# Performance work log

Hardware: AMD Instinct MI355X
Metric: run time of the kernel (lower is better)

The kernel has to match this reference:

```python
import jax, jax.numpy as jnp
import numpy as np

# TDNN with context [-2, 2], full_context=True -> kernel_width 5.
# The original per-timestep index_select + tiny conv1d loop is, for full context,
# exactly a single VALID 1D convolution over time, followed by ReLU.

B, T, D_IN, D_OUT, KW = 32, 1024, 512, 512, 5


def setup_inputs() -> dict:
    key = jax.random.key(0)
    k1, k2, k3 = jax.random.split(key, 3)
    stdv = 1.0 / np.sqrt(D_IN)
    x = jax.random.normal(k1, (B, T, D_IN), dtype=jnp.float32)
    kernel = jax.random.normal(k2, (D_OUT, D_IN, KW), dtype=jnp.float32) * stdv
    bias = jax.random.normal(k3, (D_OUT,), dtype=jnp.float32) * stdv
    return {"x": x, "kernel": kernel, "bias": bias}


def reference(x, kernel, bias):
    # x: [B, T, D_in] -> [B, D_in, T] to match torch conv1d layout
    xc = jnp.transpose(x, (0, 2, 1))
    # VALID conv over time; kernel layout OIW matches torch (out, in, width)
    out = jax.lax.conv_general_dilated(
        xc, kernel,
        window_strides=(1,),
        padding="VALID",
        dimension_numbers=("NCW", "OIW", "NCW"),
    )  # [B, D_out, T - KW + 1]
    out = out + bias[None, :, None]
    return jax.nn.relu(out)
```

## Files before the change

kernel.cpp:

```cpp
#include <hip/hip_runtime.h>
#include <stdint.h>

#define BATCH 32
#define TLEN  1024
#define DIN   512
#define DOUT  512
#define KW    5
#define TOUT  1020
#define KDIM  (DIN * KW)

#define BM 256
#define BN 256
#define BK 64
#define NT (KDIM / BK)
#define TILE_E (BM * BK)

typedef __attribute__((ext_vector_type(8))) short bf16x8;
typedef __attribute__((ext_vector_type(4))) float f32x4;

__device__ __forceinline__ uint16_t f2bf(float f) {
    uint32_t u = __float_as_uint(f);
    uint32_t r = u + 0x7FFFu + ((u >> 16) & 1u);
    return (uint16_t)(r >> 16);
}

__global__ void __launch_bounds__(256)
convert_pack(const float4* __restrict__ x, uint4* __restrict__ xb,
             const float* __restrict__ w, uint16_t* __restrict__ wb) {
    const int tid = threadIdx.x;

    for (int u = blockIdx.x; u < 8192; u += 1024) {
        int idx = u * 256 + tid;
        float4 a = x[2 * idx];
        float4 b = x[2 * idx + 1];
        uint4 v;
        v.x = (uint32_t)f2bf(a.x) | ((uint32_t)f2bf(a.y) << 16);
        v.y = (uint32_t)f2bf(a.z) | ((uint32_t)f2bf(a.w) << 16);
        v.z = (uint32_t)f2bf(b.x) | ((uint32_t)f2bf(b.y) << 16);
        v.w = (uint32_t)f2bf(b.z) | ((uint32_t)f2bf(b.w) << 16);
        xb[idx] = v;
    }

    __shared__ float4 lw4[320];
    float* lw = (float*)lw4;
    const int o = blockIdx.x >> 1;
    const int h = blockIdx.x & 1;
    const float4* src = (const float4*)(w + (size_t)o * KDIM + h * 1280);
    #pragma unroll
    for (int j = tid; j < 320; j += 256) lw4[j] = src[j];
    __syncthreads();
    #pragma unroll
    for (int k = 0; k < KW; ++k)
        wb[(size_t)o * KDIM + k * DIN + h * 256 + tid] = f2bf(lw[tid * 5 + k]);
}


#define STAGE_A(buf_, mh_, kt_) do {                                           \
    const uint16_t* lb_ = As_ + (buf_) * TILE_E + (mh_) * 8192;                \
    _Pragma("unroll")                                                          \
    for (int ii = 0; ii < 2; ++ii) {                                          \
        int c_  = ii * 512 + w * 64 + lane;                                   \
        int rh_ = c_ >> 3;                                                    \
        int g_  = (c_ & 7) ^ (rh_ & 7);                                       \
        int gr_ = ((rh_ >> 6) << 7) + (mh_) * 64 + (rh_ & 63);                \
        const uint16_t* gp_ = xrow + (size_t)gr_ * DIN + (kt_) * BK + g_ * 8; \
        const uint16_t* lp_ = lb_ + (ii * 512 + w * 64) * 8;                  \
        __builtin_amdgcn_global_load_lds(                                     \
            (const __attribute__((address_space(1))) void*)gp_,               \
            (__attribute__((address_space(3))) void*)lp_, 16, 0, 0);          \
    }                                                                          \
} while (0)

#define STAGE_B(buf_, nh_, kt_) do {                                           \
    const uint16_t* lb_ = Bs_ + (buf_) * TILE_E + (nh_) * 8192;                \
    _Pragma("unroll")                                                          \
    for (int ii = 0; ii < 2; ++ii) {                                          \
        int c_  = ii * 512 + w * 64 + lane;                                   \
        int rh_ = c_ >> 3;                                                    \
        int g_  = (c_ & 7) ^ (rh_ & 7);                                       \
        int gr_ = ((rh_ >> 5) << 6) + (nh_) * 32 + (rh_ & 31);                \
        const uint16_t* gp_ = wrow + (size_t)gr_ * KDIM + (kt_) * BK + g_ * 8;\
        const uint16_t* lp_ = lb_ + (ii * 512 + w * 64) * 8;                  \
        __builtin_amdgcn_global_load_lds(                                     \
            (const __attribute__((address_space(1))) void*)gp_,               \
            (__attribute__((address_space(3))) void*)lp_, 16, 0, 0);          \
    }                                                                          \
} while (0)

#define LDA(buf_, mh_) do {                                                    \
    const uint16_t* Ab_ = As_ + (buf_) * TILE_E;                               \
    _Pragma("unroll")                                                          \
    for (int mi = 0; mi < 4; ++mi) {                                          \
        int r_ = (mh_) * 128 + wm * 64 + mi * 16 + ml;                        \
        _Pragma("unroll")                                                      \
        for (int h2 = 0; h2 < 2; ++h2) {                                     \
            int cc_ = h2 * 4 + kg;                                            \
            af[mi][h2] = *(const bf16x8*)&Ab_[r_ * BK + ((cc_ ^ (r_ & 7)) * 8)];\
        }                                                                      \
    }                                                                          \
} while (0)

#define LDB(buf_, nh_) do {                                                    \
    const uint16_t* Bb_ = Bs_ + (buf_) * TILE_E;                               \
    _Pragma("unroll")                                                          \
    for (int ni = 0; ni < 2; ++ni) {                                          \
        int r_ = (nh_) * 128 + wn * 32 + ni * 16 + ml;                        \
        _Pragma("unroll")                                                      \
        for (int h2 = 0; h2 < 2; ++h2) {                                     \
            int cc_ = h2 * 4 + kg;                                            \
            bfr[ni][h2] = *(const bf16x8*)&Bb_[r_ * BK + ((cc_ ^ (r_ & 7)) * 8)];\
        }                                                                      \
    }                                                                          \
} while (0)

#define MMA(mh_, nh_) do {                                                     \
    _Pragma("unroll")                                                          \
    for (int h2 = 0; h2 < 2; ++h2)                                            \
        _Pragma("unroll")                                                      \
        for (int mi = 0; mi < 4; ++mi)                                        \
            _Pragma("unroll")                                                  \
            for (int ni = 0; ni < 2; ++ni)                                    \
                acc[(mh_) * 4 + mi][(nh_) * 2 + ni] =                         \
                    __builtin_amdgcn_mfma_f32_16x16x32_bf16(                  \
                        af[mi][h2], bfr[ni][h2],                              \
                        acc[(mh_) * 4 + mi][(nh_) * 2 + ni], 0, 0, 0);        \
} while (0)

#define BARW() do {                                                            \
    __builtin_amdgcn_s_barrier();                                              \
    asm volatile("s_waitcnt lgkmcnt(0)" ::: "memory");                         \
    __builtin_amdgcn_sched_barrier(0);                                         \
} while (0)

#define DO_KTILE(BUF, KT_B, GB, KT_A, GA, VM6)                                 \
       \
    LDA(BUF, 0); LDB(BUF, 0);                                                  \
    if (GB) STAGE_B(1 - (BUF), 0, KT_B);                                       \
    asm volatile("s_waitcnt lgkmcnt(8)" ::: "memory");                         \
    BARW();                                                                    \
    __builtin_amdgcn_s_setprio(1); MMA(0, 0); __builtin_amdgcn_s_setprio(0);   \
    __builtin_amdgcn_s_barrier();                                              \
                                                              \
    LDB(BUF, 1);                                                               \
    if (GA) STAGE_A(BUF, 0, KT_A);                                             \
    BARW();                                                                    \
    __builtin_amdgcn_s_setprio(1); MMA(0, 1); __builtin_amdgcn_s_setprio(0);   \
    __builtin_amdgcn_s_barrier();                                              \
                                                              \
    LDA(BUF, 1);                                                               \
    if (GA) STAGE_B(BUF, 1, KT_A);                                             \
    BARW();                                                                    \
    __builtin_amdgcn_s_setprio(1); MMA(1, 1); __builtin_amdgcn_s_setprio(0);   \
    __builtin_amdgcn_s_barrier();                                              \
                                                              \
    LDB(BUF, 0);                                                               \
    if (GA) STAGE_A(BUF, 1, KT_A);                                             \
    BARW();                                                                    \
    __builtin_amdgcn_s_setprio(1); MMA(1, 0); __builtin_amdgcn_s_setprio(0);   \
    if (VM6) { asm volatile("s_waitcnt vmcnt(6)" ::: "memory"); }              \
    else     { asm volatile("s_waitcnt vmcnt(0)" ::: "memory"); }              \
    __builtin_amdgcn_s_barrier();                                              \
    __builtin_amdgcn_sched_barrier(0);

__global__ void __launch_bounds__(512, 2)
tdnn_gemm(const uint16_t* __restrict__ xb,
          const uint16_t* __restrict__ wb,
          const float* __restrict__ bias,
          float* __restrict__ out) {
    __shared__ uint16_t As_[2 * TILE_E];
    __shared__ uint16_t Bs_[2 * TILE_E];

    const int j  = blockIdx.x;
    const int g  = (j & 7) * 32 + (j >> 3);
    const int mt = g >> 1;
    const int nt = g & 1;
    const int b  = mt >> 2;
    const int t0 = (mt & 3) * BM;
    const int n0 = nt * BN;

    const int tid  = threadIdx.x;
    const int lane = tid & 63;
    const int w    = tid >> 6;
    const int wm   = w >> 2;
    const int wn   = w & 3;
    const int ml   = lane & 15;
    const int kg   = lane >> 4;

    const uint16_t* xrow = xb + (size_t)b * TLEN * DIN + (size_t)t0 * DIN;
    const uint16_t* wrow = wb + (size_t)n0 * KDIM;

    f32x4 acc[8][4] = {};
    bf16x8 af[4][2];
    bf16x8 bfr[2][2];

    STAGE_A(0, 0, 0);
    STAGE_B(0, 0, 0);
    STAGE_A(0, 1, 0);
    STAGE_B(0, 1, 0);
    STAGE_A(1, 0, 1);
    STAGE_B(1, 1, 1);
    STAGE_A(1, 1, 1);
    asm volatile("s_waitcnt vmcnt(6)" ::: "memory");
    __builtin_amdgcn_s_barrier();
    __builtin_amdgcn_sched_barrier(0);

    for (int kt = 0; kt < NT; kt += 2) {
        const bool ga0 = (kt + 2) < NT;
        const bool ga1 = (kt + 3) < NT;
        DO_KTILE(0, kt + 1, true, kt + 2, ga0, ga0)
        DO_KTILE(1, kt + 2, ga0,  kt + 3, ga1, ga1)
    }

    const int rq = (lane >> 4) * 4;
    #pragma unroll
    for (int nf = 0; nf < 4; ++nf) {
        const int o = n0 + wn * 64 + (nf >> 1) * 32 + (nf & 1) * 16 + ml;
        const float bv = bias[o];
        float* orow = out + ((size_t)b * DOUT + o) * TOUT;
        #pragma unroll
        for (int mf = 0; mf < 8; ++mf) {
            const int tb_ = t0 + wm * 128 + (mf >> 2) * 64 + (mf & 3) * 16 + rq;
            if (tb_ + 3 < TOUT) {
                float4 s;
                s.x = fmaxf(acc[mf][nf][0] + bv, 0.0f);
                s.y = fmaxf(acc[mf][nf][1] + bv, 0.0f);
                s.z = fmaxf(acc[mf][nf][2] + bv, 0.0f);
                s.w = fmaxf(acc[mf][nf][3] + bv, 0.0f);
                *(float4*)(orow + tb_) = s;
            }
        }
    }
}

extern "C" void kernel_launch(void* const* d_in, const int* in_sizes, int n_in,
                              void* d_out, int out_size, void* d_ws, size_t ws_size,
                              hipStream_t stream) {
    const float* x    = (const float*)d_in[0];
    const float* wgt  = (const float*)d_in[1];
    const float* bias = (const float*)d_in[2];
    float* out = (float*)d_out;

    uint16_t* xb = (uint16_t*)d_ws;
    uint16_t* wb = (uint16_t*)((char*)d_ws + (size_t)BATCH * TLEN * DIN * 2);

    convert_pack<<<1024, 256, 0, stream>>>((const float4*)x, (uint4*)xb, wgt, wb);
    tdnn_gemm<<<256, 512, 0, stream>>>(xb, wb, bias, out);
}
```

Before: 198.4 us.

## Load weight fragments directly from global into registers, keep only activations in LDS

Weight (B) tiles no longer go through shared memory. Each wave now loads its B fragments straight from global memory into registers. A tiles are still staged in LDS through global_load_lds, with hoisted precomputed addresses and separate A-fragment register sets, and the pipeline is rewritten with an explicit peeled epilogue and retuned vmcnt/lgkmcnt waits. This halves LDS footprint and LDS traffic, which may allow more occupancy and fewer barriers. The cost is uncoalesced, strided global reads of weights per wave, with more register pressure and a higher risk of exposed global latency.

```diff
diff --git a/kernel.cpp b/kernel.cpp
--- a/kernel.cpp
+++ b/kernel.cpp
@@ -13,7 +13,7 @@
 #define BN 256
 #define BK 64
 #define NT (KDIM / BK)
-#define TILE_E (BM * BK)
+#define ATILE_E (BM * BK)
 
 typedef __attribute__((ext_vector_type(8))) short bf16x8;
 typedef __attribute__((ext_vector_type(4))) float f32x4;
@@ -28,7 +28,6 @@
 convert_pack(const float4* __restrict__ x, uint4* __restrict__ xb,
              const float* __restrict__ w, uint16_t* __restrict__ wb) {
     const int tid = threadIdx.x;
-
     for (int u = blockIdx.x; u < 8192; u += 1024) {
         int idx = u * 256 + tid;
         float4 a = x[2 * idx];
@@ -40,7 +39,6 @@
         v.w = (uint32_t)f2bf(b.z) | ((uint32_t)f2bf(b.w) << 16);
         xb[idx] = v;
     }
-
     __shared__ float4 lw4[320];
     float* lw = (float*)lw4;
     const int o = blockIdx.x >> 1;
@@ -55,120 +53,96 @@
 }
 
 
-#define STAGE_A(buf_, mh_, kt_) do {                                           \
-    const uint16_t* lb_ = As_ + (buf_) * TILE_E + (mh_) * 8192;                \
-    _Pragma("unroll")                                                          \
-    for (int ii = 0; ii < 2; ++ii) {                                          \
-        int c_  = ii * 512 + w * 64 + lane;                                   \
-        int rh_ = c_ >> 3;                                                    \
-        int g_  = (c_ & 7) ^ (rh_ & 7);                                       \
-        int gr_ = ((rh_ >> 6) << 7) + (mh_) * 64 + (rh_ & 63);                \
-        const uint16_t* gp_ = xrow + (size_t)gr_ * DIN + (kt_) * BK + g_ * 8; \
-        const uint16_t* lp_ = lb_ + (ii * 512 + w * 64) * 8;                  \
-        __builtin_amdgcn_global_load_lds(                                     \
-            (const __attribute__((address_space(1))) void*)gp_,               \
-            (__attribute__((address_space(3))) void*)lp_, 16, 0, 0);          \
+#define SB() __builtin_amdgcn_sched_barrier(0)
+#define BAR() do { __builtin_amdgcn_s_barrier(); SB(); } while (0)
+#define WAITVM(N) do { asm volatile("s_waitcnt vmcnt(" #N ")" ::: "memory"); SB(); } while (0)
+#define WAITLG(N) do { asm volatile("s_waitcnt lgkmcnt(" #N ")" ::: "memory"); SB(); } while (0)
+
+#define STAGE_A(BUF_, MH_, KT_) do {                                           \
+    _Pragma("unroll")                                                          \
+    for (int ii = 0; ii < 2; ++ii) {                                           \
+        const uint16_t* gp_ = xrow + ab + (MH_) * 32768 + ii * 65536 + (KT_) * 64; \
+        const uint16_t* lp_ = As_ + (BUF_) * ATILE_E + (MH_) * 8192 + ii * 4096 + w * 512; \
+        __builtin_amdgcn_global_load_lds(                                      \
+            (const __attribute__((address_space(1))) void*)gp_,                \
+            (__attribute__((address_space(3))) void*)lp_, 16, 0, 0);           \
     }                                                                          \
 } while (0)
 
-#define STAGE_B(buf_, nh_, kt_) do {                                           \
-    const uint16_t* lb_ = Bs_ + (buf_) * TILE_E + (nh_) * 8192;                \
-    _Pragma("unroll")                                                          \
-    for (int ii = 0; ii < 2; ++ii) {                                          \
-        int c_  = ii * 512 + w * 64 + lane;                                   \
-        int rh_ = c_ >> 3;                                                    \
-        int g_  = (c_ & 7) ^ (rh_ & 7);                                       \
-        int gr_ = ((rh_ >> 5) << 6) + (nh_) * 32 + (rh_ & 31);                \
-        const uint16_t* gp_ = wrow + (size_t)gr_ * KDIM + (kt_) * BK + g_ * 8;\
-        const uint16_t* lp_ = lb_ + (ii * 512 + w * 64) * 8;                  \
-        __builtin_amdgcn_global_load_lds(                                     \
-            (const __attribute__((address_space(1))) void*)gp_,               \
-            (__attribute__((address_space(3))) void*)lp_, 16, 0, 0);          \
+#define DS_AFA(SRC_) do {                                                      \
+    _Pragma("unroll")                                                          \
+    for (int mi = 0; mi < 4; ++mi) {                                           \
+        afA[mi][0] = *(const bf16x8*)&As_[(SRC_) * ATILE_E + mi * 1024 + ae0]; \
+        afA[mi][1] = *(const bf16x8*)&As_[(SRC_) * ATILE_E + mi * 1024 + ae1]; \
     }                                                                          \
 } while (0)
 
-#define LDA(buf_, mh_) do {                                                    \
-    const uint16_t* Ab_ = As_ + (buf_) * TILE_E;                               \
-    _Pragma("unroll")                                                          \
-    for (int mi = 0; mi < 4; ++mi) {                                          \
-        int r_ = (mh_) * 128 + wm * 64 + mi * 16 + ml;                        \
+#define DS_AFB(SRC_) do {                                                      \
+    _Pragma("unroll")                                                          \
+    for (int mi = 0; mi < 4; ++mi) {                                           \
+        afB[mi][0] = *(const bf16x8*)&As_[(SRC_) * ATILE_E + 8192 + mi * 1024 + ae0]; \
+        afB[mi][1] = *(const bf16x8*)&As_[(SRC_) * ATILE_E + 8192 + mi * 1024 + ae1]; \
+    }                                                                          \
+} while (0)
+
+#define GLB_B0(KT_) do {                                                       \
+    bf0[0][0] = *(const bf16x8*)(wrow + bo00 + (KT_) * 64);                    \
+    bf0[0][1] = *(const bf16x8*)(wrow + bo00 + (KT_) * 64 + 32);               \
+    bf0[1][0] = *(const bf16x8*)(wrow + bo01 + (KT_) * 64);                    \
+    bf0[1][1] = *(const bf16x8*)(wrow + bo01 + (KT_) * 64 + 32);               \
+} while (0)
+
+#define GLB_B1(KT_) do {                                                       \
+    bf1[0][0] = *(const bf16x8*)(wrow + bo10 + (KT_) * 64);                    \
+    bf1[0][1] = *(const bf16x8*)(wrow + bo10 + (KT_) * 64 + 32);               \
+    bf1[1][0] = *(const bf16x8*)(wrow + bo11 + (KT_) * 64);                    \
+    bf1[1][1] = *(const bf16x8*)(wrow + bo11 + (KT_) * 64 + 32);               \
+} while (0)
+
+#define MMA(MH_, NH_, AF_, BF_) do {                                           \
+    __builtin_amdgcn_s_setprio(1);                                             \
+    _Pragma("unroll")                                                          \
+    for (int h2 = 0; h2 < 2; ++h2)                                             \
         _Pragma("unroll")                                                      \
-        for (int h2 = 0; h2 < 2; ++h2) {                                     \
-            int cc_ = h2 * 4 + kg;                                            \
-            af[mi][h2] = *(const bf16x8*)&Ab_[r_ * BK + ((cc_ ^ (r_ & 7)) * 8)];\
-        }                                                                      \
-    }                                                                          \
-} while (0)
-
-#define LDB(buf_, nh_) do {                                                    \
-    const uint16_t* Bb_ = Bs_ + (buf_) * TILE_E;                               \
-    _Pragma("unroll")                                                          \
-    for (int ni = 0; ni < 2; ++ni) {                                          \
-        int r_ = (nh_) * 128 + wn * 32 + ni * 16 + ml;                        \
-        _Pragma("unroll")                                                      \
-        for (int h2 = 0; h2 < 2; ++h2) {                                     \
-            int cc_ = h2 * 4 + kg;                                            \
-            bfr[ni][h2] = *(const bf16x8*)&Bb_[r_ * BK + ((cc_ ^ (r_ & 7)) * 8)];\
-        }                                                                      \
-    }                                                                          \
-} while (0)
-
-#define MMA(mh_, nh_) do {                                                     \
-    _Pragma("unroll")                                                          \
-    for (int h2 = 0; h2 < 2; ++h2)                                            \
-        _Pragma("unroll")                                                      \
-        for (int mi = 0; mi < 4; ++mi)                                        \
+        for (int mi = 0; mi < 4; ++mi)                                         \
             _Pragma("unroll")                                                  \
-            for (int ni = 0; ni < 2; ++ni)                                    \
-                acc[(mh_) * 4 + mi][(nh_) * 2 + ni] =                         \
-                    __builtin_amdgcn_mfma_f32_16x16x32_bf16(                  \
-                        af[mi][h2], bfr[ni][h2],                              \
-                        acc[(mh_) * 4 + mi][(nh_) * 2 + ni], 0, 0, 0);        \
-} while (0)
-
-#define BARW() do {                                                            \
-    __builtin_amdgcn_s_barrier();                                              \
-    asm volatile("s_waitcnt lgkmcnt(0)" ::: "memory");                         \
-    __builtin_amdgcn_sched_barrier(0);                                         \
-} while (0)
-
-#define DO_KTILE(BUF, KT_B, GB, KT_A, GA, VM6)                                 \
-       \
-    LDA(BUF, 0); LDB(BUF, 0);                                                  \
-    if (GB) STAGE_B(1 - (BUF), 0, KT_B);                                       \
-    asm volatile("s_waitcnt lgkmcnt(8)" ::: "memory");                         \
-    BARW();                                                                    \
-    __builtin_amdgcn_s_setprio(1); MMA(0, 0); __builtin_amdgcn_s_setprio(0);   \
-    __builtin_amdgcn_s_barrier();                                              \
-                                                              \
-    LDB(BUF, 1);                                                               \
-    if (GA) STAGE_A(BUF, 0, KT_A);                                             \
-    BARW();                                                                    \
-    __builtin_amdgcn_s_setprio(1); MMA(0, 1); __builtin_amdgcn_s_setprio(0);   \
-    __builtin_amdgcn_s_barrier();                                              \
-                                                              \
-    LDA(BUF, 1);                                                               \
-    if (GA) STAGE_B(BUF, 1, KT_A);                                             \
-    BARW();                                                                    \
-    __builtin_amdgcn_s_setprio(1); MMA(1, 1); __builtin_amdgcn_s_setprio(0);   \
-    __builtin_amdgcn_s_barrier();                                              \
-                                                              \
-    LDB(BUF, 0);                                                               \
-    if (GA) STAGE_A(BUF, 1, KT_A);                                             \
-    BARW();                                                                    \
-    __builtin_amdgcn_s_setprio(1); MMA(1, 0); __builtin_amdgcn_s_setprio(0);   \
-    if (VM6) { asm volatile("s_waitcnt vmcnt(6)" ::: "memory"); }              \
-    else     { asm volatile("s_waitcnt vmcnt(0)" ::: "memory"); }              \
-    __builtin_amdgcn_s_barrier();                                              \
-    __builtin_amdgcn_sched_barrier(0);
+            for (int ni = 0; ni < 2; ++ni)                                     \
+                acc[(MH_) * 4 + mi][(NH_) * 2 + ni] =                          \
+                    __builtin_amdgcn_mfma_f32_16x16x32_bf16(                   \
+                        AF_[mi][h2], BF_[ni][h2],                              \
+                        acc[(MH_) * 4 + mi][(NH_) * 2 + ni], 0, 0, 0);         \
+    __builtin_amdgcn_s_setprio(0);                                             \
+} while (0)
+
+#define TILE_STEADY(BUF_, KT_)                                                 \
+                                                                      \
+    GLB_B1(KT_);                                                               \
+    WAITVM(6); WAITLG(0);                                                      \
+    MMA(0, 0, afA, bf0);                                                       \
+    BAR();                                                                     \
+                                                                      \
+    STAGE_A(BUF_, 0, (KT_) + 2);                                               \
+    WAITVM(2);                                                                 \
+    DS_AFB(BUF_);                                                              \
+    MMA(0, 1, afA, bf1);                                                       \
+    BAR();                                                                     \
+                                                                      \
+    DS_AFA(1 - (BUF_));                                                        \
+    WAITLG(8);                                                                 \
+    MMA(1, 1, afB, bf1);                                                       \
+    BAR();                                                                     \
+                                                                      \
+    STAGE_A(BUF_, 1, (KT_) + 2);                                               \
+    MMA(1, 0, afB, bf0);                                                       \
+    GLB_B0((KT_) + 1);                                                         \
+    SB();
 
 __global__ void __launch_bounds__(512, 2)
 tdnn_gemm(const uint16_t* __restrict__ xb,
           const uint16_t* __restrict__ wb,
           const float* __restrict__ bias,
           float* __restrict__ out) {
-    __shared__ uint16_t As_[2 * TILE_E];
-    __shared__ uint16_t Bs_[2 * TILE_E];
+    __shared__ uint16_t As_[2 * ATILE_E];
 
     const int j  = blockIdx.x;
     const int g  = (j & 7) * 32 + (j >> 3);
@@ -189,27 +163,63 @@
     const uint16_t* xrow = xb + (size_t)b * TLEN * DIN + (size_t)t0 * DIN;
     const uint16_t* wrow = wb + (size_t)n0 * KDIM;
 
+    const int rh0 = (w * 64 + lane) >> 3;
+    const int gsw = (lane & 7) ^ ((w * 8 + (lane >> 3)) & 7);
+    const int ab  = rh0 * DIN + gsw * 8;
+
+    const int ae0 = wm * 4096 + ml * 64 + ((kg)     ^ (ml & 7)) * 8;
+    const int ae1 = wm * 4096 + ml * 64 + ((4 + kg) ^ (ml & 7)) * 8;
+
+    const int bo00 = (wn * 64 +  0 + ml) * KDIM + kg * 8;
+    const int bo01 = (wn * 64 + 16 + ml) * KDIM + kg * 8;
+    const int bo10 = (wn * 64 + 32 + ml) * KDIM + kg * 8;
+    const int bo11 = (wn * 64 + 48 + ml) * KDIM + kg * 8;
+
     f32x4 acc[8][4] = {};
-    bf16x8 af[4][2];
-    bf16x8 bfr[2][2];
+    bf16x8 afA[4][2], afB[4][2];
+    bf16x8 bf0[2][2], bf1[2][2];
 
     STAGE_A(0, 0, 0);
-    STAGE_B(0, 0, 0);
     STAGE_A(0, 1, 0);
-    STAGE_B(0, 1, 0);
     STAGE_A(1, 0, 1);
-    STAGE_B(1, 1, 1);
+    GLB_B0(0);
     STAGE_A(1, 1, 1);
-    asm volatile("s_waitcnt vmcnt(6)" ::: "memory");
-    __builtin_amdgcn_s_barrier();
-    __builtin_amdgcn_sched_barrier(0);
-
-    for (int kt = 0; kt < NT; kt += 2) {
-        const bool ga0 = (kt + 2) < NT;
-        const bool ga1 = (kt + 3) < NT;
-        DO_KTILE(0, kt + 1, true, kt + 2, ga0, ga0)
-        DO_KTILE(1, kt + 2, ga0,  kt + 3, ga1, ga1)
+    WAITVM(8);
+    BAR();
+    DS_AFA(0);
+
+    for (int kt = 0; kt < 38; kt += 2) {
+        TILE_STEADY(0, kt)
+        TILE_STEADY(1, kt + 1)
     }
+
+    GLB_B1(38);
+    WAITVM(6); WAITLG(0);
+    MMA(0, 0, afA, bf0);
+    BAR();
+    WAITVM(0);
+    DS_AFB(0);
+    MMA(0, 1, afA, bf1);
+    BAR();
+    DS_AFA(1);
+    WAITLG(8);
+    MMA(1, 1, afB, bf1);
+    BAR();
+    MMA(1, 0, afB, bf0);
+    GLB_B0(39);
+    SB();
+
+    GLB_B1(39);
+    WAITVM(4); WAITLG(0);
+    MMA(0, 0, afA, bf0);
+    BAR();
+    WAITVM(0);
+    DS_AFB(1);
+    MMA(0, 1, afA, bf1);
+    BAR();
+    WAITLG(0);
+    MMA(1, 1, afB, bf1);
+    MMA(1, 0, afB, bf0);
 
     const int rq = (lane >> 4) * 4;
     #pragma unroll
```

New measurement: 246.2 us. 24.1% more time.
